# Kernel optimization log

Measured on AMD Instinct MI355X. Metric: run time of the kernel, lower is better.

Reference implementation:

```python
import jax, jax.numpy as jnp
import numpy as np

FORMULA_OH_SIZES = [20, 20, 20, 20, 20]
SPECT_BIN_N = 512


def layer_norm(x, g, b, eps=1e-5):
    m = jnp.mean(x, axis=-1, keepdims=True)
    v = jnp.var(x, axis=-1, keepdims=True)
    return (x - m) * jax.lax.rsqrt(v + eps) * g + b


def gru_cell(x, h, W_ih, W_hh, b_ih, b_hh):
    # torch.nn.GRUCell math
    gi = x @ W_ih.T + b_ih
    gh = h @ W_hh.T + b_hh
    i_r, i_z, i_n = jnp.split(gi, 3, axis=-1)
    h_r, h_z, h_n = jnp.split(gh, 3, axis=-1)
    r = jax.nn.sigmoid(i_r + h_r)
    z = jax.nn.sigmoid(i_z + h_z)
    n = jnp.tanh(i_n + r * h_n)
    return (1.0 - z) * n + z * h


def structured_one_hot(x, sizes, accum=True):
    # x: [N, len(sizes)] integer element counts -> concatenated (accumulated) one-hots
    outs = []
    for i, s in enumerate(sizes):
        v = jnp.clip(x[:, i].astype(jnp.int32), 0, s - 1)
        if accum:
            oh = (jnp.arange(s)[None, :] <= v[:, None]).astype(jnp.float32)  # thermometer
        else:
            oh = jax.nn.one_hot(v, s, dtype=jnp.float32)
        outs.append(oh)
    return jnp.concatenate(outs, axis=-1)


def setup_inputs():
    key = jax.random.key(0)
    ks = jax.random.split(key, 16)
    B, A, GF, HW, S, M = 16, 32, 128, 4, 4096, 8
    G = GF * HW                       # 512 = g_feat_in * highway_steps_n
    FE = sum(FORMULA_OH_SIZES)        # 100
    D = 512                           # internal_d
    vert_feat_in = jax.random.normal(ks[0], (B, A, GF, HW), jnp.float32)
    vert_mask_in = jnp.ones((B, A), jnp.float32)
    elem_id = jax.random.randint(ks[1], (B, A), 0, 5)
    vert_element_oh = jax.nn.one_hot(elem_id, 5, dtype=jnp.float32)
    adj_oh = jnp.zeros((B, A, A, 4), jnp.float32)  # unused by forward
    atom_subsets = jax.random.bernoulli(ks[2], 0.5, (B, S, A)).astype(jnp.float32)
    masses = jax.random.uniform(ks[3], (B, S, M), jnp.float32, 0.0, SPECT_BIN_N - 1.0)
    intens = jax.random.uniform(ks[4], (B, S, M), jnp.float32)
    atom_subsets_peaks = jnp.stack([masses, intens], axis=-1)

    def lin(k, o, i):
        return (jax.random.normal(k, (o, i), jnp.float32) / np.sqrt(i)).astype(jnp.float32)

    return dict(
        vert_feat_in=vert_feat_in, vert_mask_in=vert_mask_in,
        vert_element_oh=vert_element_oh, adj_oh=adj_oh,
        atom_subsets=atom_subsets, atom_subsets_peaks=atom_subsets_peaks,
        ln_sub_g=jnp.ones((G,), jnp.float32), ln_sub_b=jnp.zeros((G,), jnp.float32),
        W_ih=lin(ks[5], 3 * G, FE), W_hh=lin(ks[6], 3 * G, G),
        b_ih=jnp.zeros((3 * G,), jnp.float32), b_hh=jnp.zeros((3 * G,), jnp.float32),
        W1=lin(ks[7], D, G), b1=jnp.zeros((D,), jnp.float32),
        W2a=lin(ks[8], D, D), b2a=jnp.zeros((D,), jnp.float32),
        W2b=lin(ks[9], D, D), b2b=jnp.zeros((D,), jnp.float32),
        ln_pre_g=jnp.ones((D,), jnp.float32), ln_pre_b=jnp.zeros((D,), jnp.float32),
        Ws=lin(ks[10], 1, D), bs=jnp.zeros((1,), jnp.float32),
    )


def reference(vert_feat_in, vert_mask_in, vert_element_oh, adj_oh, atom_subsets,
              atom_subsets_peaks, ln_sub_g, ln_sub_b, W_ih, W_hh, b_ih, b_hh,
              W1, b1, W2a, b2a, W2b, b2b, ln_pre_g, ln_pre_b, Ws, bs):
    B, A, GF, HW = vert_feat_in.shape
    S = atom_subsets.shape[1]
    vf = vert_feat_in.reshape(B, A, GF * HW)                       # [B,A,G]
    masked_vf = vf * vert_mask_in[:, :, None]
    subs_m = atom_subsets * vert_mask_in[:, None, :]               # [B,S,A]
    swvs = jnp.einsum('bag,bsa->bsg', masked_vf, subs_m)           # [B,S,G]
    # per-subset element counts -> structured one-hot formula encoding
    counts = jnp.einsum('bae,bsa->bse', vert_element_oh, atom_subsets).astype(jnp.int32)
    pf_flat = structured_one_hot(counts.reshape(B * S, -1), FORMULA_OH_SIZES, accum=True)
    subset_size = jnp.sum(subs_m, axis=2) + 1e-4                   # [B,S]
    mean = swvs / subset_size[:, :, None]
    normed = layer_norm(mean, ln_sub_g, ln_sub_b)                  # [B,S,G]
    h = gru_cell(pf_flat, normed.reshape(B * S, -1), W_ih, W_hh, b_ih, b_hh)
    h = h.reshape(normed.shape)
    x = jax.nn.relu(h @ W1.T + b1)
    x = jax.nn.relu(x @ W2a.T + b2a)
    x = jax.nn.relu(x @ W2b.T + b2b)   # (extra F.relu in original is idempotent)
    x = layer_norm(x, ln_pre_g, ln_pre_b)
    scores = (x @ Ws.T + bs)[..., 0]                               # [B,S]
    probs = jax.nn.softmax(scores, axis=-1)
    # mass histogram: scatter intensity*prob into rounded-mass bins
    masses = atom_subsets_peaks[..., 0]                            # [B,S,M]
    intens = atom_subsets_peaks[..., 1]
    bins = jnp.clip(jnp.round(masses).astype(jnp.int32), 0, SPECT_BIN_N - 1)
    contrib = intens * probs[:, :, None]                           # [B,S,M]
    spect = jnp.zeros((B, SPECT_BIN_N), x.dtype).at[
        jnp.arange(B)[:, None], bins.reshape(B, -1)].add(contrib.reshape(B, -1))
    return (spect, probs)
```

## Files before the change

kernel.cpp:

```cpp
#include <hip/hip_runtime.h>
#include <math.h>

#define B_ 16
#define A_ 32
#define G_ 512
#define S_ 4096
#define M_ 8
#define BS_ 65536
#define KC_ 640
#define NG_ 1536

typedef _Float16 half8 __attribute__((ext_vector_type(8)));
typedef _Float16 half4v __attribute__((ext_vector_type(4)));
typedef _Float16 half2v __attribute__((ext_vector_type(2)));
typedef float floatx4 __attribute__((ext_vector_type(4)));

typedef const __attribute__((address_space(1))) void* gas_t;
typedef __attribute__((address_space(3))) void* las_t;

__device__ __forceinline__ float wave_sum_f(float v){
#pragma unroll
  for (int o = 32; o > 0; o >>= 1) v += __shfl_xor(v, o);
  return v;
}
__device__ __forceinline__ float wave_max_f(float v){
#pragma unroll
  for (int o = 32; o > 0; o >>= 1) v = fmaxf(v, __shfl_xor(v, o));
  return v;
}
__device__ __forceinline__ float sigmoidf_(float x){ return 1.f/(1.f+__expf(-x)); }
__device__ __forceinline__ float tanhf_(float x){ return 1.f - 2.f/(__expf(2.f*x)+1.f); }

__global__ __launch_bounds__(256) void k_cvt(const float* __restrict__ s,
                                             _Float16* __restrict__ d, int n){
  int i = (blockIdx.x*256 + threadIdx.x)*4;
  if (i >= n) return;
  float4 v = *(const float4*)(s+i);
  half4v o; o[0]=(_Float16)v.x; o[1]=(_Float16)v.y; o[2]=(_Float16)v.z; o[3]=(_Float16)v.w;
  *(half4v*)(d+i) = o;
}

__global__ __launch_bounds__(64) void k_buildw(const float* __restrict__ Whh,
                                               const float* __restrict__ Wih,
                                               _Float16* __restrict__ Wcat){
  int j = blockIdx.x;
  for (int p = threadIdx.x; p < KC_; p += 64){
    float v = 0.f;
    if (p < 512) v = Whh[(size_t)j*512 + p];
    else if (p < 612 && j < 1024) v = Wih[(size_t)j*100 + (p - 512)];
    Wcat[(size_t)j*KC_ + p] = (_Float16)v;
  }
}

__global__ __launch_bounds__(256) void k_pn(const float* __restrict__ Wih,
                                            float* __restrict__ Pn){
  int d = blockIdx.x*256 + threadIdx.x;
  if (d >= 512) return;
  const float* src = Wih + (size_t)(1024 + d)*100;
#pragma unroll
  for (int f = 0; f < 5; ++f){
    int off = f*20;
    float run = 0.f;
    for (int k = 0; k < 20; ++k){
      run += src[off + k];
      Pn[(size_t)(off + k)*512 + d] = run;
    }
  }
}

__global__ __launch_bounds__(256) void k_prep_mfma(
    const float* __restrict__ vf, const float* __restrict__ mask,
    const float* __restrict__ eoh, const float* __restrict__ subs,
    const float* __restrict__ ln_g, const float* __restrict__ ln_b,
    _Float16* __restrict__ Abuf, int* __restrict__ cpk){
  __shared__ _Float16 s_mvfT[G_*A_];
  __shared__ _Float16 s_sm[128*A_];
  __shared__ float s_m[A_];
  __shared__ float s_e[A_*5];
  __shared__ float s_ssum[128];
  __shared__ float s_red1[4][16];
  __shared__ float s_red2[4][16];
  int tid = threadIdx.x;
  int bx = blockIdx.x, b = blockIdx.y;
  int lane = tid & 63, w = tid >> 6;
  int q = lane >> 4, l15 = lane & 15;
  size_t row0 = (size_t)b*S_ + (size_t)bx*128;
  if (tid < A_)   s_m[tid] = mask[b*A_ + tid];
  if (tid < A_*5) s_e[tid] = eoh[b*A_*5 + tid];
  __syncthreads();
  {
    int p = tid & 15, gseg = tid >> 4;
    float mk0 = s_m[2*p], mk1 = s_m[2*p+1];
    const float* v0 = vf + ((size_t)b*A_ + 2*p)*G_ + gseg*32;
    const float* v1 = v0 + G_;
#pragma unroll
    for (int i = 0; i < 32; ++i){
      int g = gseg*32 + i;
      half2v h; h[0] = (_Float16)(v0[i]*mk0); h[1] = (_Float16)(v1[i]*mk1);
      *(half2v*)(s_mvfT + g*A_ + 2*p) = h;
    }
  }
  {
    int s = tid >> 1, hh = tid & 1;
    const float* sp = subs + (row0 + s)*A_ + hh*16;
#pragma unroll
    for (int i = 0; i < 16; i += 2){
      half2v h; h[0] = (_Float16)sp[i]; h[1] = (_Float16)sp[i+1];
      *(half2v*)(s_sm + s*A_ + hh*16 + i) = h;
    }
  }
  __syncthreads();
  if (tid < 128){
    int s = tid;
    float ssum = 0.f, c0=0.f, c1=0.f, c2=0.f, c3=0.f, c4=0.f;
#pragma unroll
    for (int a = 0; a < A_; ++a){
      float v = (float)s_sm[s*A_ + a];
      ssum += v * s_m[a];
      c0 += v * s_e[a*5+0]; c1 += v * s_e[a*5+1]; c2 += v * s_e[a*5+2];
      c3 += v * s_e[a*5+3]; c4 += v * s_e[a*5+4];
    }
    int cc[5];
    cc[0] = min(max((int)(c0+0.5f),0),19); cc[1] = min(max((int)(c1+0.5f),0),19);
    cc[2] = min(max((int)(c2+0.5f),0),19); cc[3] = min(max((int)(c3+0.5f),0),19);
    cc[4] = min(max((int)(c4+0.5f),0),19);
    cpk[row0 + s] = cc[0] | (cc[1]<<6) | (cc[2]<<12) | (cc[3]<<18) | (cc[4]<<24);
    s_ssum[s] = ssum;
    _Float16* dst = Abuf + (row0 + s)*KC_ + 512;
#pragma unroll
    for (int t = 0; t < 16; ++t){
      half8 hv;
#pragma unroll
      for (int u = 0; u < 8; ++u){
        int k = t*8 + u;
        float v = 0.f;
        if (k < 100){ int f = k/20, l = k - f*20; v = (l <= cc[f]) ? 1.f : 0.f; }
        hv[u] = (_Float16)v;
      }
      *(half8*)(dst + t*8) = hv;
    }
  }
  half8 bf[8]; float lng[8], lnb[8];
#pragma unroll
  for (int t = 0; t < 8; ++t){
    int g = w*128 + t*16 + l15;
    bf[t] = *(const half8*)(s_mvfT + g*A_ + q*8);
    lng[t] = ln_g[g]; lnb[t] = ln_b[g];
  }
  __syncthreads();
  for (int gi = 0; gi < 8; ++gi){
    half8 af = *(const half8*)(s_sm + (gi*16 + l15)*A_ + q*8);
    floatx4 c[8];
#pragma unroll
    for (int t = 0; t < 8; ++t){
      floatx4 z = {0.f, 0.f, 0.f, 0.f};
      c[t] = __builtin_amdgcn_mfma_f32_16x16x32_f16(af, bf[t], z, 0, 0, 0);
    }
    float p1[4] = {0.f,0.f,0.f,0.f}, p2[4] = {0.f,0.f,0.f,0.f};
#pragma unroll
    for (int t = 0; t < 8; ++t)
#pragma unroll
      for (int r = 0; r < 4; ++r){ float v = c[t][r]; p1[r] += v; p2[r] += v*v; }
#pragma unroll
    for (int off = 1; off < 16; off <<= 1)
#pragma unroll
      for (int r = 0; r < 4; ++r){
        p1[r] += __shfl_xor(p1[r], off);
        p2[r] += __shfl_xor(p2[r], off);
      }
    if (l15 == 0){
#pragma unroll
      for (int r = 0; r < 4; ++r){ s_red1[w][q*4+r] = p1[r]; s_red2[w][q*4+r] = p2[r]; }
    }
    __syncthreads();
#pragma unroll
    for (int r = 0; r < 4; ++r){
      int sl = gi*16 + q*4 + r;
      int rr = q*4 + r;
      float t1 = s_red1[0][rr] + s_red1[1][rr] + s_red1[2][rr] + s_red1[3][rr];
      float t2 = s_red2[0][rr] + s_red2[1][rr] + s_red2[2][rr] + s_red2[3][rr];
      float inv = 1.f/(s_ssum[sl] + 1e-4f);
      float mu = t1*inv*(1.f/512.f);
      float var = t2*inv*inv*(1.f/512.f) - mu*mu;
      float rs = rsqrtf(var + 1e-5f);
      _Float16* orow = Abuf + (row0 + sl)*KC_;
#pragma unroll
      for (int t = 0; t < 8; ++t){
        float o = (c[t][r]*inv - mu)*rs*lng[t] + lnb[t];
        orow[w*128 + t*16 + l15] = (_Float16)o;
      }
    }
    __syncthreads();
  }
}

__global__ __launch_bounds__(512) void k_gru_fused(
    const _Float16* __restrict__ Abuf, const _Float16* __restrict__ Wcat,
    const float* __restrict__ Pn, const float* __restrict__ bih,
    const float* __restrict__ bhh, const int* __restrict__ cpk,
    _Float16* __restrict__ H){
  __shared__ _Float16 smA[128*32];
  __shared__ _Float16 smB[192*32];
  int tid = threadIdx.x;
  int lane = tid & 63, wvid = tid >> 6;
  int wm = wvid & 1, wn = wvid >> 1;
  int q = lane >> 4, l15 = lane & 15;
  int mt = blockIdx.x*64 + (blockIdx.y >> 3);
  int dt = blockIdx.y & 7;
  int m0 = mt*128, n0 = dt*64;
  floatx4 acc[3][4] = {};
  int offA[4], offB[3];
#pragma unroll
  for (int i = 0; i < 4; ++i){
    int r = wm*64 + i*16 + l15;
    offA[i] = (r*4 + (q ^ ((r>>2)&3)))*8;
  }
#pragma unroll
  for (int g = 0; g < 3; ++g){
    int rb = g*64 + wn*16 + l15;
    offB[g] = (rb*4 + (q ^ ((rb>>2)&3)))*8;
  }
  const _Float16* gA;
  {
    int u = wvid*64 + lane;
    int r = u >> 2, c = (u & 3) ^ ((r >> 2) & 3);
    gA = Abuf + (size_t)(m0 + r)*KC_ + c*8;
  }
  const _Float16* gB0;
  {
    int u = wvid*64 + lane;
    int rb = u >> 2, c = (u & 3) ^ ((rb >> 2) & 3);
    int grow = (rb >> 6)*512 + n0 + (rb & 63);
    gB0 = Wcat + (size_t)grow*KC_ + c*8;
  }
  const _Float16* gB1 = nullptr;
  if (wvid < 4){
    int u = (8 + wvid)*64 + lane;
    int rb = u >> 2, c = (u & 3) ^ ((rb >> 2) & 3);
    int grow = (rb >> 6)*512 + n0 + (rb & 63);
    gB1 = Wcat + (size_t)grow*KC_ + c*8;
  }
  for (int kc = 0; kc < KC_; kc += 32){
    __builtin_amdgcn_global_load_lds((gas_t)(gA + kc), (las_t)(smA + wvid*512), 16, 0, 0);
    __builtin_amdgcn_global_load_lds((gas_t)(gB0 + kc), (las_t)(smB + wvid*512), 16, 0, 0);
    if (wvid < 4)
      __builtin_amdgcn_global_load_lds((gas_t)(gB1 + kc), (las_t)(smB + (8+wvid)*512), 16, 0, 0);
    __syncthreads();
    half8 af[4], bfv[3];
#pragma unroll
    for (int i = 0; i < 4; ++i) af[i] = *(const half8*)(smA + offA[i]);
#pragma unroll
    for (int g = 0; g < 3; ++g) bfv[g] = *(const half8*)(smB + offB[g]);
#pragma unroll
    for (int g = 0; g < 3; ++g)
#pragma unroll
      for (int i = 0; i < 4; ++i)
        acc[g][i] = __builtin_amdgcn_mfma_f32_16x16x32_f16(af[i], bfv[g], acc[g][i], 0, 0, 0);
    __syncthreads();
  }
  int d = n0 + wn*16 + l15;
  float br  = bih[d] + bhh[d];
  float bz  = bih[512+d] + bhh[512+d];
  float bnh = bhh[1024+d];
  float bni = bih[1024+d];
#pragma unroll
  for (int i = 0; i < 4; ++i){
#pragma unroll
    for (int r = 0; r < 4; ++r){
      int m = m0 + wm*64 + i*16 + q*4 + r;
      int cp = cpk[m];
      int k0 =  (cp      ) & 63;
      int k1 = ((cp >> 6 ) & 63) + 20;
      int k2 = ((cp >> 12) & 63) + 40;
      int k3 = ((cp >> 18) & 63) + 60;
      int k4 = ((cp >> 24) & 63) + 80;
      float in_ = bni + Pn[(size_t)k0*512 + d] + Pn[(size_t)k1*512 + d]
                + Pn[(size_t)k2*512 + d] + Pn[(size_t)k3*512 + d]
                + Pn[(size_t)k4*512 + d];
      float gr = acc[0][i][r] + br;
      float gz = acc[1][i][r] + bz;
      float hn = acc[2][i][r] + bnh;
      float rrv = sigmoidf_(gr);
      float zz  = sigmoidf_(gz);
      float nn  = tanhf_(in_ + rrv*hn);
      float hp = (float)Abuf[(size_t)m*KC_ + d];
      H[(size_t)m*G_ + d] = (_Float16)((1.f-zz)*nn + zz*hp);
    }
  }
}

__global__ __launch_bounds__(256) void k_gemm(
    const _Float16* __restrict__ A, const _Float16* __restrict__ W,
    const float* __restrict__ bias, _Float16* __restrict__ Out){
  __shared__ _Float16 smA[128*32];
  __shared__ _Float16 smB[128*32];
  int tid = threadIdx.x;
  int lane = tid & 63, wvid = tid >> 6;
  int wm = wvid & 1, wn = wvid >> 1;
  int q = lane >> 4, l15 = lane & 15;
  int mt = blockIdx.x*64 + (blockIdx.y >> 2);
  int nt = blockIdx.y & 3;
  int m0 = mt*128, n0 = nt*128;
  floatx4 acc[4][4] = {};
  int offA[4], offB[4];
#pragma unroll
  for (int i = 0; i < 4; ++i){
    int r = wm*64 + i*16 + l15;
    offA[i] = (r*4 + (q ^ ((r>>2)&3)))*8;
    int rb = wn*64 + i*16 + l15;
    offB[i] = (rb*4 + (q ^ ((rb>>2)&3)))*8;
  }
  int uA[2];
  const _Float16 *gA[2], *gB[2];
#pragma unroll
  for (int t = 0; t < 2; ++t){
    int seg = wvid*2 + t;
    int u = seg*64 + lane;
    int r = u >> 2, c = (u & 3) ^ ((r >> 2) & 3);
    uA[t] = seg;
    gA[t] = A + (size_t)(m0 + r)*G_ + c*8;
    gB[t] = W + (size_t)(n0 + r)*G_ + c*8;
  }
  for (int kc = 0; kc < G_; kc += 32){
#pragma unroll
    for (int t = 0; t < 2; ++t){
      __builtin_amdgcn_global_load_lds((gas_t)(gA[t] + kc), (las_t)(smA + uA[t]*512), 16, 0, 0);
      __builtin_amdgcn_global_load_lds((gas_t)(gB[t] + kc), (las_t)(smB + uA[t]*512), 16, 0, 0);
    }
    __syncthreads();
    half8 af[4], bfv[4];
#pragma unroll
    for (int i = 0; i < 4; ++i) af[i] = *(const half8*)(smA + offA[i]);
#pragma unroll
    for (int j = 0; j < 4; ++j) bfv[j] = *(const half8*)(smB + offB[j]);
#pragma unroll
    for (int i = 0; i < 4; ++i)
#pragma unroll
      for (int j = 0; j < 4; ++j)
        acc[i][j] = __builtin_amdgcn_mfma_f32_16x16x32_f16(af[i], bfv[j], acc[i][j], 0, 0, 0);
    __syncthreads();
  }
#pragma unroll
  for (int j = 0; j < 4; ++j){
    int n = n0 + wn*64 + j*16 + l15;
    float bv = bias[n];
#pragma unroll
    for (int i = 0; i < 4; ++i){
#pragma unroll
      for (int r = 0; r < 4; ++r){
        int m = m0 + wm*64 + i*16 + q*4 + r;
        Out[(size_t)m*G_ + n] = (_Float16)fmaxf(acc[i][j][r] + bv, 0.f);
      }
    }
  }
}

__global__ __launch_bounds__(256) void k_ln_score(
    const _Float16* __restrict__ X, const float* __restrict__ g,
    const float* __restrict__ bta, const float* __restrict__ Ws,
    const float* __restrict__ bs, float* __restrict__ scores){
  int tid = threadIdx.x, lane = tid & 63, wv = tid >> 6;
  size_t row0 = (size_t)blockIdx.x*32 + wv*8;
  int e0 = lane*8;
  float wv_[8], gv[8], bv[8];
  *(float4*)(wv_ ) = *(const float4*)(Ws + e0);
  *(float4*)(wv_+4) = *(const float4*)(Ws + e0 + 4);
  *(float4*)(gv  ) = *(const float4*)(g + e0);
  *(float4*)(gv+4) = *(const float4*)(g + e0 + 4);
  *(float4*)(bv  ) = *(const float4*)(bta + e0);
  *(float4*)(bv+4) = *(const float4*)(bta + e0 + 4);
  float bsv = bs[0];
  for (int rr = 0; rr < 8; ++rr){
    size_t row = row0 + rr;
    half8 hx = *(const half8*)(X + row*G_ + e0);
    float xv[8];
#pragma unroll
    for (int t = 0; t < 8; ++t) xv[t] = (float)hx[t];
    float s1 = 0.f, s2 = 0.f;
#pragma unroll
    for (int t = 0; t < 8; ++t){ s1 += xv[t]; s2 += xv[t]*xv[t]; }
    s1 = wave_sum_f(s1); s2 = wave_sum_f(s2);
    float mu = s1*(1.f/512.f);
    float var = s2*(1.f/512.f) - mu*mu;
    float rs = rsqrtf(var + 1e-5f);
    float sc = 0.f;
#pragma unroll
    for (int t = 0; t < 8; ++t) sc += ((xv[t]-mu)*rs*gv[t] + bv[t])*wv_[t];
    sc = wave_sum_f(sc);
    if (lane == 0) scores[row] = sc + bsv;
  }
}

__global__ __launch_bounds__(256) void k_softmax(
    const float* __restrict__ scores, float* __restrict__ probs){
  __shared__ float red[4];
  int b = blockIdx.x, tid = threadIdx.x, lane = tid & 63, wv = tid >> 6;
  const float* sp = scores + (size_t)b*S_;
  float mx = -1e30f;
  for (int i = tid; i < S_; i += 256) mx = fmaxf(mx, sp[i]);
  mx = wave_max_f(mx);
  if (lane == 0) red[wv] = mx;
  __syncthreads();
  mx = fmaxf(fmaxf(red[0], red[1]), fmaxf(red[2], red[3]));
  __syncthreads();
  float sum = 0.f;
  for (int i = tid; i < S_; i += 256) sum += __expf(sp[i]-mx);
  sum = wave_sum_f(sum);
  if (lane == 0) red[wv] = sum;
  __syncthreads();
  sum = red[0]+red[1]+red[2]+red[3];
  float inv = 1.f/sum;
  for (int i = tid; i < S_; i += 256)
    probs[(size_t)b*S_ + i] = __expf(sp[i]-mx)*inv;
}

__global__ __launch_bounds__(256) void k_spect(
    const float* __restrict__ peaks, const float* __restrict__ probs,
    float* __restrict__ spect){
  __shared__ float bins[512];
  int b = blockIdx.x, tid = threadIdx.x;
  bins[tid] = 0.f; bins[tid+256] = 0.f;
  __syncthreads();
  for (int i = tid; i < S_*M_; i += 256){
    int s = i >> 3, m = i & 7;
    const float* pk = peaks + (((size_t)b*S_ + s)*M_ + m)*2;
    float mass = pk[0], inten = pk[1];
    float p = probs[(size_t)b*S_ + s];
    int bin = (int)rintf(mass);
    bin = min(max(bin, 0), 511);
    atomicAdd(&bins[bin], inten*p);
  }
  __syncthreads();
  spect[(size_t)b*512 + tid]       = bins[tid];
  spect[(size_t)b*512 + tid + 256] = bins[tid+256];
}

extern "C" void kernel_launch(void* const* d_in, const int* in_sizes, int n_in,
                              void* d_out, int out_size, void* d_ws, size_t ws_size,
                              hipStream_t stream) {
  const float* vf       = (const float*)d_in[0];
  const float* mask     = (const float*)d_in[1];
  const float* eoh      = (const float*)d_in[2];
  const float* subs     = (const float*)d_in[4];
  const float* peaks    = (const float*)d_in[5];
  const float* ln_sub_g = (const float*)d_in[6];
  const float* ln_sub_b = (const float*)d_in[7];
  const float* W_ih     = (const float*)d_in[8];
  const float* W_hh     = (const float*)d_in[9];
  const float* b_ih     = (const float*)d_in[10];
  const float* b_hh     = (const float*)d_in[11];
  const float* W1       = (const float*)d_in[12];
  const float* b1       = (const float*)d_in[13];
  const float* W2a      = (const float*)d_in[14];
  const float* b2a      = (const float*)d_in[15];
  const float* W2b      = (const float*)d_in[16];
  const float* b2b      = (const float*)d_in[17];
  const float* ln_pre_g = (const float*)d_in[18];
  const float* ln_pre_b = (const float*)d_in[19];
  const float* Ws       = (const float*)d_in[20];
  const float* bs       = (const float*)d_in[21];
  float* out = (float*)d_out;
  float* probs_out = out + (size_t)B_*512;

  char* w = (char*)d_ws;
  float* Pn = (float*)w;         w += (size_t)100*512*4;
  int*   cpk = (int*)w;          w += (size_t)BS_*4;
  float* scores = (float*)w;     w += (size_t)BS_*4;
  _Float16* Wcat = (_Float16*)w; w += (size_t)NG_*KC_*2;
  _Float16* W1h  = (_Float16*)w; w += (size_t)G_*G_*2;
  _Float16* W2ah = (_Float16*)w; w += (size_t)G_*G_*2;
  _Float16* W2bh = (_Float16*)w; w += (size_t)G_*G_*2;
  _Float16* Abuf = (_Float16*)w; w += (size_t)BS_*KC_*2;
  _Float16* bufh0 = (_Float16*)w;
  _Float16* bufh1 = Abuf;

  k_cvt<<<(G_*G_/4+255)/256, 256, 0, stream>>>(W1,  W1h,  G_*G_);
  k_cvt<<<(G_*G_/4+255)/256, 256, 0, stream>>>(W2a, W2ah, G_*G_);
  k_cvt<<<(G_*G_/4+255)/256, 256, 0, stream>>>(W2b, W2bh, G_*G_);
  k_buildw<<<NG_, 64, 0, stream>>>(W_hh, W_ih, Wcat);
  k_pn<<<2, 256, 0, stream>>>(W_ih, Pn);
  k_prep_mfma<<<dim3(S_/128, B_), 256, 0, stream>>>(vf, mask, eoh, subs,
                                                    ln_sub_g, ln_sub_b, Abuf, cpk);
  k_gru_fused<<<dim3(8, 512), 512, 0, stream>>>(Abuf, Wcat, Pn, b_ih, b_hh,
                                                cpk, bufh0);
  k_gemm<<<dim3(8, 256), 256, 0, stream>>>(bufh0, W1h,  b1,  bufh1);
  k_gemm<<<dim3(8, 256), 256, 0, stream>>>(bufh1, W2ah, b2a, bufh0);
  k_gemm<<<dim3(8, 256), 256, 0, stream>>>(bufh0, W2bh, b2b, bufh1);
  k_ln_score<<<BS_/32, 256, 0, stream>>>(bufh1, ln_pre_g, ln_pre_b, Ws, bs, scores);
  k_softmax<<<B_, 256, 0, stream>>>(scores, probs_out);
  k_spect<<<B_, 256, 0, stream>>>(peaks, probs_out, out);
}
```

Measured before the change: 541.6 us.

## Switch GRU and MLP GEMMs to 32x32x16 MFMA with larger per-wave tiles

Replaces the 16x16x32 MFMA tiling in the fused GRU kernel and the MLP GEMM kernel with 32x32x16 instructions, so each wave now computes 64x32 or 64x64 output tiles. The LDS swizzle is changed to suit the new fragment read pattern. The GRU kernel drops from 512 to 256 threads per block, with each wave loading more segments. The aim is fewer LDS fragment reads per FLOP and higher MFMA throughput, at the cost of more accumulator registers per wave and a changed epilogue row mapping.

```diff
diff --git a/kernel.cpp b/kernel.cpp
--- a/kernel.cpp
+++ b/kernel.cpp
@@ -14,6 +14,7 @@
 typedef _Float16 half4v __attribute__((ext_vector_type(4)));
 typedef _Float16 half2v __attribute__((ext_vector_type(2)));
 typedef float floatx4 __attribute__((ext_vector_type(4)));
+typedef float floatx16 __attribute__((ext_vector_type(16)));
 
 typedef const __attribute__((address_space(1))) void* gas_t;
 typedef __attribute__((address_space(3))) void* las_t;
@@ -194,7 +195,7 @@
   }
 }
 
-__global__ __launch_bounds__(512) void k_gru_fused(
+__global__ __launch_bounds__(256) void k_gru_fused(
     const _Float16* __restrict__ Abuf, const _Float16* __restrict__ Wcat,
     const float* __restrict__ Pn, const float* __restrict__ bih,
     const float* __restrict__ bhh, const int* __restrict__ cpk,
@@ -204,70 +205,81 @@
   int tid = threadIdx.x;
   int lane = tid & 63, wvid = tid >> 6;
   int wm = wvid & 1, wn = wvid >> 1;
-  int q = lane >> 4, l15 = lane & 15;
+  int l31 = lane & 31, lhi = lane >> 5;
   int mt = blockIdx.x*64 + (blockIdx.y >> 3);
   int dt = blockIdx.y & 7;
   int m0 = mt*128, n0 = dt*64;
-  floatx4 acc[3][4] = {};
-  int offA[4], offB[3];
-#pragma unroll
-  for (int i = 0; i < 4; ++i){
-    int r = wm*64 + i*16 + l15;
-    offA[i] = (r*4 + (q ^ ((r>>2)&3)))*8;
+  floatx16 acc[3][2] = {};
+  int offA[2][2], offB[3][2];
+#pragma unroll
+  for (int mi = 0; mi < 2; ++mi){
+    int r = wm*64 + mi*32 + l31;
+#pragma unroll
+    for (int c = 0; c < 2; ++c)
+      offA[mi][c] = (r*4 + ((c*2 + lhi) ^ ((r>>1)&3)))*8;
   }
 #pragma unroll
   for (int g = 0; g < 3; ++g){
-    int rb = g*64 + wn*16 + l15;
-    offB[g] = (rb*4 + (q ^ ((rb>>2)&3)))*8;
-  }
-  const _Float16* gA;
-  {
-    int u = wvid*64 + lane;
-    int r = u >> 2, c = (u & 3) ^ ((r >> 2) & 3);
-    gA = Abuf + (size_t)(m0 + r)*KC_ + c*8;
-  }
-  const _Float16* gB0;
-  {
-    int u = wvid*64 + lane;
-    int rb = u >> 2, c = (u & 3) ^ ((rb >> 2) & 3);
+    int rb = g*64 + wn*32 + l31;
+#pragma unroll
+    for (int c = 0; c < 2; ++c)
+      offB[g][c] = (rb*4 + ((c*2 + lhi) ^ ((rb>>1)&3)))*8;
+  }
+  const _Float16* gA[2]; int sAo[2];
+#pragma unroll
+  for (int t = 0; t < 2; ++t){
+    int seg = wvid + t*4;
+    int u = seg*64 + lane;
+    int r = u >> 2, c = (u & 3) ^ ((r >> 1) & 3);
+    gA[t] = Abuf + (size_t)(m0 + r)*KC_ + c*8;
+    sAo[t] = seg*512;
+  }
+  const _Float16* gB[3]; int sBo[3];
+#pragma unroll
+  for (int t = 0; t < 3; ++t){
+    int seg = wvid*3 + t;
+    int u = seg*64 + lane;
+    int rb = u >> 2, c = (u & 3) ^ ((rb >> 1) & 3);
     int grow = (rb >> 6)*512 + n0 + (rb & 63);
-    gB0 = Wcat + (size_t)grow*KC_ + c*8;
-  }
-  const _Float16* gB1 = nullptr;
-  if (wvid < 4){
-    int u = (8 + wvid)*64 + lane;
-    int rb = u >> 2, c = (u & 3) ^ ((rb >> 2) & 3);
-    int grow = (rb >> 6)*512 + n0 + (rb & 63);
-    gB1 = Wcat + (size_t)grow*KC_ + c*8;
+    gB[t] = Wcat + (size_t)grow*KC_ + c*8;
+    sBo[t] = seg*512;
   }
   for (int kc = 0; kc < KC_; kc += 32){
-    __builtin_amdgcn_global_load_lds((gas_t)(gA + kc), (las_t)(smA + wvid*512), 16, 0, 0);
-    __builtin_amdgcn_global_load_lds((gas_t)(gB0 + kc), (las_t)(smB + wvid*512), 16, 0, 0);
-    if (wvid < 4)
-      __builtin_amdgcn_global_load_lds((gas_t)(gB1 + kc), (las_t)(smB + (8+wvid)*512), 16, 0, 0);
+#pragma unroll
+    for (int t = 0; t < 2; ++t)
+      __builtin_amdgcn_global_load_lds((gas_t)(gA[t] + kc), (las_t)(smA + sAo[t]), 16, 0, 0);
+#pragma unroll
+    for (int t = 0; t < 3; ++t)
+      __builtin_amdgcn_global_load_lds((gas_t)(gB[t] + kc), (las_t)(smB + sBo[t]), 16, 0, 0);
     __syncthreads();
-    half8 af[4], bfv[3];
-#pragma unroll
-    for (int i = 0; i < 4; ++i) af[i] = *(const half8*)(smA + offA[i]);
-#pragma unroll
-    for (int g = 0; g < 3; ++g) bfv[g] = *(const half8*)(smB + offB[g]);
+    half8 af[2][2], bfv[3][2];
+#pragma unroll
+    for (int mi = 0; mi < 2; ++mi)
+#pragma unroll
+      for (int c = 0; c < 2; ++c) af[mi][c] = *(const half8*)(smA + offA[mi][c]);
 #pragma unroll
     for (int g = 0; g < 3; ++g)
 #pragma unroll
-      for (int i = 0; i < 4; ++i)
-        acc[g][i] = __builtin_amdgcn_mfma_f32_16x16x32_f16(af[i], bfv[g], acc[g][i], 0, 0, 0);
+      for (int c = 0; c < 2; ++c) bfv[g][c] = *(const half8*)(smB + offB[g][c]);
+#pragma unroll
+    for (int g = 0; g < 3; ++g)
+#pragma unroll
+      for (int mi = 0; mi < 2; ++mi)
+#pragma unroll
+        for (int c = 0; c < 2; ++c)
+          acc[g][mi] = __builtin_amdgcn_mfma_f32_32x32x16_f16(af[mi][c], bfv[g][c], acc[g][mi], 0, 0, 0);
     __syncthreads();
   }
-  int d = n0 + wn*16 + l15;
+  int d = n0 + wn*32 + l31;
   float br  = bih[d] + bhh[d];
   float bz  = bih[512+d] + bhh[512+d];
   float bnh = bhh[1024+d];
   float bni = bih[1024+d];
 #pragma unroll
-  for (int i = 0; i < 4; ++i){
-#pragma unroll
-    for (int r = 0; r < 4; ++r){
-      int m = m0 + wm*64 + i*16 + q*4 + r;
+  for (int mi = 0; mi < 2; ++mi){
+#pragma unroll
+    for (int rr = 0; rr < 16; ++rr){
+      int m = m0 + wm*64 + mi*32 + (rr&3) + 8*(rr>>2) + 4*lhi;
       int cp = cpk[m];
       int k0 =  (cp      ) & 63;
       int k1 = ((cp >> 6 ) & 63) + 20;
@@ -277,9 +289,9 @@
       float in_ = bni + Pn[(size_t)k0*512 + d] + Pn[(size_t)k1*512 + d]
                 + Pn[(size_t)k2*512 + d] + Pn[(size_t)k3*512 + d]
                 + Pn[(size_t)k4*512 + d];
-      float gr = acc[0][i][r] + br;
-      float gz = acc[1][i][r] + bz;
-      float hn = acc[2][i][r] + bnh;
+      float gr = acc[0][mi][rr] + br;
+      float gz = acc[1][mi][rr] + bz;
+      float hn = acc[2][mi][rr] + bnh;
       float rrv = sigmoidf_(gr);
       float zz  = sigmoidf_(gz);
       float nn  = tanhf_(in_ + rrv*hn);
@@ -297,59 +309,66 @@
   int tid = threadIdx.x;
   int lane = tid & 63, wvid = tid >> 6;
   int wm = wvid & 1, wn = wvid >> 1;
-  int q = lane >> 4, l15 = lane & 15;
+  int l31 = lane & 31, lhi = lane >> 5;
   int mt = blockIdx.x*64 + (blockIdx.y >> 2);
   int nt = blockIdx.y & 3;
   int m0 = mt*128, n0 = nt*128;
-  floatx4 acc[4][4] = {};
-  int offA[4], offB[4];
-#pragma unroll
-  for (int i = 0; i < 4; ++i){
-    int r = wm*64 + i*16 + l15;
-    offA[i] = (r*4 + (q ^ ((r>>2)&3)))*8;
-    int rb = wn*64 + i*16 + l15;
-    offB[i] = (rb*4 + (q ^ ((rb>>2)&3)))*8;
-  }
-  int uA[2];
-  const _Float16 *gA[2], *gB[2];
+  floatx16 acc[2][2] = {};
+  int offA[2][2], offB[2][2];
+#pragma unroll
+  for (int mi = 0; mi < 2; ++mi){
+    int r = wm*64 + mi*32 + l31;
+    int rb = wn*64 + mi*32 + l31;
+#pragma unroll
+    for (int c = 0; c < 2; ++c){
+      offA[mi][c] = (r*4 + ((c*2 + lhi) ^ ((r>>1)&3)))*8;
+      offB[mi][c] = (rb*4 + ((c*2 + lhi) ^ ((rb>>1)&3)))*8;
+    }
+  }
+  const _Float16 *gA[2], *gB[2]; int uo[2];
 #pragma unroll
   for (int t = 0; t < 2; ++t){
     int seg = wvid*2 + t;
     int u = seg*64 + lane;
-    int r = u >> 2, c = (u & 3) ^ ((r >> 2) & 3);
-    uA[t] = seg;
+    int r = u >> 2, c = (u & 3) ^ ((r >> 1) & 3);
+    uo[t] = seg*512;
     gA[t] = A + (size_t)(m0 + r)*G_ + c*8;
     gB[t] = W + (size_t)(n0 + r)*G_ + c*8;
   }
   for (int kc = 0; kc < G_; kc += 32){
 #pragma unroll
     for (int t = 0; t < 2; ++t){
-      __builtin_amdgcn_global_load_lds((gas_t)(gA[t] + kc), (las_t)(smA + uA[t]*512), 16, 0, 0);
-      __builtin_amdgcn_global_load_lds((gas_t)(gB[t] + kc), (las_t)(smB + uA[t]*512), 16, 0, 0);
+      __builtin_amdgcn_global_load_lds((gas_t)(gA[t] + kc), (las_t)(smA + uo[t]), 16, 0, 0);
+      __builtin_amdgcn_global_load_lds((gas_t)(gB[t] + kc), (las_t)(smB + uo[t]), 16, 0, 0);
     }
     __syncthreads();
-    half8 af[4], bfv[4];
-#pragma unroll
-    for (int i = 0; i < 4; ++i) af[i] = *(const half8*)(smA + offA[i]);
-#pragma unroll
-    for (int j = 0; j < 4; ++j) bfv[j] = *(const half8*)(smB + offB[j]);
-#pragma unroll
-    for (int i = 0; i < 4; ++i)
-#pragma unroll
-      for (int j = 0; j < 4; ++j)
-        acc[i][j] = __builtin_amdgcn_mfma_f32_16x16x32_f16(af[i], bfv[j], acc[i][j], 0, 0, 0);
+    half8 af[2][2], bfv[2][2];
+#pragma unroll
+    for (int mi = 0; mi < 2; ++mi)
+#pragma unroll
+      for (int c = 0; c < 2; ++c){
+        af[mi][c] = *(const half8*)(smA + offA[mi][c]);
+        bfv[mi][c] = *(const half8*)(smB + offB[mi][c]);
+      }
+#pragma unroll
+    for (int mi = 0; mi < 2; ++mi)
+#pragma unroll
+      for (int nj = 0; nj < 2; ++nj)
+#pragma unroll
+        for (int c = 0; c < 2; ++c)
+          acc[mi][nj] = __builtin_amdgcn_mfma_f32_32x32x16_f16(af[mi][c], bfv[nj][c], acc[mi][nj], 0, 0, 0);
     __syncthreads();
   }
 #pragma unroll
-  for (int j = 0; j < 4; ++j){
-    int n = n0 + wn*64 + j*16 + l15;
+  for (int nj = 0; nj < 2; ++nj){
+    int n = n0 + wn*64 + nj*32 + l31;
     float bv = bias[n];
 #pragma unroll
-    for (int i = 0; i < 4; ++i){
-#pragma unroll
-      for (int r = 0; r < 4; ++r){
-        int m = m0 + wm*64 + i*16 + q*4 + r;
-        Out[(size_t)m*G_ + n] = (_Float16)fmaxf(acc[i][j][r] + bv, 0.f);
+    for (int mi = 0; mi < 2; ++mi){
+#pragma unroll
+      for (int rr = 0; rr < 16; ++rr){
+        int m = m0 + wm*64 + mi*32 + (rr&3) + 8*(rr>>2) + 4*lhi;
+        Out[(size_t)m*G_ + n] = (_Float16)fmaxf(acc[mi][nj][rr] + bv, 0.f);
       }
     }
   }
@@ -481,7 +500,7 @@
   k_pn<<<2, 256, 0, stream>>>(W_ih, Pn);
   k_prep_mfma<<<dim3(S_/128, B_), 256, 0, stream>>>(vf, mask, eoh, subs,
                                                     ln_sub_g, ln_sub_b, Abuf, cpk);
-  k_gru_fused<<<dim3(8, 512), 512, 0, stream>>>(Abuf, Wcat, Pn, b_ih, b_hh,
+  k_gru_fused<<<dim3(8, 512), 256, 0, stream>>>(Abuf, Wcat, Pn, b_ih, b_hh,
                                                 cpk, bufh0);
   k_gemm<<<dim3(8, 256), 256, 0, stream>>>(bufh0, W1h,  b1,  bufh1);
   k_gemm<<<dim3(8, 256), 256, 0, stream>>>(bufh1, W2ah, b2a, bufh0);
```

New measurement: 567.2 us. 1.05x slower.

## Replace one-hot input GEMM columns with prefix-sum table lookups for all gates

Applied to the files above, without the earlier changes.

The GRU input contribution from the thermometer one-hot formula encoding was folded into the GEMM as 128 extra K columns (K=640). It is now computed for all three gates by gathering five entries from per-gate prefix-sum tables of W_ih. This shrinks the GEMM K dimension to 512, drops the one-hot writes in the prep kernel, and replaces the weight-concat kernel with a plain conversion. In exchange the epilogue does 15 scattered table loads per output element instead of 5, which may add cache pressure.

```diff
diff --git a/kernel.cpp b/kernel.cpp
--- a/kernel.cpp
+++ b/kernel.cpp
@@ -7,7 +7,6 @@
 #define S_ 4096
 #define M_ 8
 #define BS_ 65536
-#define KC_ 640
 #define NG_ 1536
 
 typedef _Float16 half8 __attribute__((ext_vector_type(8)));
@@ -40,30 +39,20 @@
   *(half4v*)(d+i) = o;
 }
 
-__global__ __launch_bounds__(64) void k_buildw(const float* __restrict__ Whh,
-                                               const float* __restrict__ Wih,
-                                               _Float16* __restrict__ Wcat){
-  int j = blockIdx.x;
-  for (int p = threadIdx.x; p < KC_; p += 64){
-    float v = 0.f;
-    if (p < 512) v = Whh[(size_t)j*512 + p];
-    else if (p < 612 && j < 1024) v = Wih[(size_t)j*100 + (p - 512)];
-    Wcat[(size_t)j*KC_ + p] = (_Float16)v;
-  }
-}
-
-__global__ __launch_bounds__(256) void k_pn(const float* __restrict__ Wih,
-                                            float* __restrict__ Pn){
-  int d = blockIdx.x*256 + threadIdx.x;
-  if (d >= 512) return;
-  const float* src = Wih + (size_t)(1024 + d)*100;
+__global__ __launch_bounds__(256) void k_pt(const float* __restrict__ Wih,
+                                            float* __restrict__ Pt){
+  int j = blockIdx.x*256 + threadIdx.x;
+  if (j >= 1536) return;
+  int g = j >> 9, d = j & 511;
+  const float* src = Wih + (size_t)j*100;
+  float* dst = Pt + (size_t)g*100*512 + d;
 #pragma unroll
   for (int f = 0; f < 5; ++f){
     int off = f*20;
     float run = 0.f;
     for (int k = 0; k < 20; ++k){
       run += src[off + k];
-      Pn[(size_t)(off + k)*512 + d] = run;
+      dst[(size_t)(off + k)*512] = run;
     }
   }
 }
@@ -126,19 +115,6 @@
     cc[4] = min(max((int)(c4+0.5f),0),19);
     cpk[row0 + s] = cc[0] | (cc[1]<<6) | (cc[2]<<12) | (cc[3]<<18) | (cc[4]<<24);
     s_ssum[s] = ssum;
-    _Float16* dst = Abuf + (row0 + s)*KC_ + 512;
-#pragma unroll
-    for (int t = 0; t < 16; ++t){
-      half8 hv;
-#pragma unroll
-      for (int u = 0; u < 8; ++u){
-        int k = t*8 + u;
-        float v = 0.f;
-        if (k < 100){ int f = k/20, l = k - f*20; v = (l <= cc[f]) ? 1.f : 0.f; }
-        hv[u] = (_Float16)v;
-      }
-      *(half8*)(dst + t*8) = hv;
-    }
   }
   half8 bf[8]; float lng[8], lnb[8];
 #pragma unroll
@@ -183,7 +159,7 @@
       float mu = t1*inv*(1.f/512.f);
       float var = t2*inv*inv*(1.f/512.f) - mu*mu;
       float rs = rsqrtf(var + 1e-5f);
-      _Float16* orow = Abuf + (row0 + sl)*KC_;
+      _Float16* orow = Abuf + (row0 + sl)*G_;
 #pragma unroll
       for (int t = 0; t < 8; ++t){
         float o = (c[t][r]*inv - mu)*rs*lng[t] + lnb[t];
@@ -195,8 +171,8 @@
 }
 
 __global__ __launch_bounds__(512) void k_gru_fused(
-    const _Float16* __restrict__ Abuf, const _Float16* __restrict__ Wcat,
-    const float* __restrict__ Pn, const float* __restrict__ bih,
+    const _Float16* __restrict__ Abuf, const _Float16* __restrict__ W16,
+    const float* __restrict__ Pt, const float* __restrict__ bih,
     const float* __restrict__ bhh, const int* __restrict__ cpk,
     _Float16* __restrict__ H){
   __shared__ _Float16 smA[128*32];
@@ -224,23 +200,23 @@
   {
     int u = wvid*64 + lane;
     int r = u >> 2, c = (u & 3) ^ ((r >> 2) & 3);
-    gA = Abuf + (size_t)(m0 + r)*KC_ + c*8;
+    gA = Abuf + (size_t)(m0 + r)*G_ + c*8;
   }
   const _Float16* gB0;
   {
     int u = wvid*64 + lane;
     int rb = u >> 2, c = (u & 3) ^ ((rb >> 2) & 3);
     int grow = (rb >> 6)*512 + n0 + (rb & 63);
-    gB0 = Wcat + (size_t)grow*KC_ + c*8;
+    gB0 = W16 + (size_t)grow*G_ + c*8;
   }
   const _Float16* gB1 = nullptr;
   if (wvid < 4){
     int u = (8 + wvid)*64 + lane;
     int rb = u >> 2, c = (u & 3) ^ ((rb >> 2) & 3);
     int grow = (rb >> 6)*512 + n0 + (rb & 63);
-    gB1 = Wcat + (size_t)grow*KC_ + c*8;
-  }
-  for (int kc = 0; kc < KC_; kc += 32){
+    gB1 = W16 + (size_t)grow*G_ + c*8;
+  }
+  for (int kc = 0; kc < G_; kc += 32){
     __builtin_amdgcn_global_load_lds((gas_t)(gA + kc), (las_t)(smA + wvid*512), 16, 0, 0);
     __builtin_amdgcn_global_load_lds((gas_t)(gB0 + kc), (las_t)(smB + wvid*512), 16, 0, 0);
     if (wvid < 4)
@@ -259,6 +235,9 @@
     __syncthreads();
   }
   int d = n0 + wn*16 + l15;
+  const float* Pr = Pt + d;
+  const float* Pz = Pt + 100*512 + d;
+  const float* Pn = Pt + 200*512 + d;
   float br  = bih[d] + bhh[d];
   float bz  = bih[512+d] + bhh[512+d];
   float bnh = bhh[1024+d];
@@ -269,21 +248,22 @@
     for (int r = 0; r < 4; ++r){
       int m = m0 + wm*64 + i*16 + q*4 + r;
       int cp = cpk[m];
-      int k0 =  (cp      ) & 63;
-      int k1 = ((cp >> 6 ) & 63) + 20;
-      int k2 = ((cp >> 12) & 63) + 40;
-      int k3 = ((cp >> 18) & 63) + 60;
-      int k4 = ((cp >> 24) & 63) + 80;
-      float in_ = bni + Pn[(size_t)k0*512 + d] + Pn[(size_t)k1*512 + d]
-                + Pn[(size_t)k2*512 + d] + Pn[(size_t)k3*512 + d]
-                + Pn[(size_t)k4*512 + d];
-      float gr = acc[0][i][r] + br;
-      float gz = acc[1][i][r] + bz;
+      int k0 = ((cp      ) & 63)*512;
+      int k1 = (((cp >> 6 ) & 63) + 20)*512;
+      int k2 = (((cp >> 12) & 63) + 40)*512;
+      int k3 = (((cp >> 18) & 63) + 60)*512;
+      int k4 = (((cp >> 24) & 63) + 80)*512;
+      float sr = Pr[k0]+Pr[k1]+Pr[k2]+Pr[k3]+Pr[k4];
+      float sz = Pz[k0]+Pz[k1]+Pz[k2]+Pz[k3]+Pz[k4];
+      float sn = Pn[k0]+Pn[k1]+Pn[k2]+Pn[k3]+Pn[k4];
+      float gr = acc[0][i][r] + br + sr;
+      float gz = acc[1][i][r] + bz + sz;
       float hn = acc[2][i][r] + bnh;
+      float in_ = bni + sn;
       float rrv = sigmoidf_(gr);
       float zz  = sigmoidf_(gz);
       float nn  = tanhf_(in_ + rrv*hn);
-      float hp = (float)Abuf[(size_t)m*KC_ + d];
+      float hp = (float)Abuf[(size_t)m*G_ + d];
       H[(size_t)m*G_ + d] = (_Float16)((1.f-zz)*nn + zz*hp);
     }
   }
@@ -463,25 +443,25 @@
   float* probs_out = out + (size_t)B_*512;
 
   char* w = (char*)d_ws;
-  float* Pn = (float*)w;         w += (size_t)100*512*4;
+  float* Pt = (float*)w;         w += (size_t)3*100*512*4;
   int*   cpk = (int*)w;          w += (size_t)BS_*4;
   float* scores = (float*)w;     w += (size_t)BS_*4;
-  _Float16* Wcat = (_Float16*)w; w += (size_t)NG_*KC_*2;
+  _Float16* W3h  = (_Float16*)w; w += (size_t)NG_*G_*2;
   _Float16* W1h  = (_Float16*)w; w += (size_t)G_*G_*2;
   _Float16* W2ah = (_Float16*)w; w += (size_t)G_*G_*2;
   _Float16* W2bh = (_Float16*)w; w += (size_t)G_*G_*2;
-  _Float16* Abuf = (_Float16*)w; w += (size_t)BS_*KC_*2;
+  _Float16* Abuf = (_Float16*)w; w += (size_t)BS_*G_*2;
   _Float16* bufh0 = (_Float16*)w;
   _Float16* bufh1 = Abuf;
 
+  k_cvt<<<(NG_*G_/4+255)/256, 256, 0, stream>>>(W_hh, W3h, NG_*G_);
   k_cvt<<<(G_*G_/4+255)/256, 256, 0, stream>>>(W1,  W1h,  G_*G_);
   k_cvt<<<(G_*G_/4+255)/256, 256, 0, stream>>>(W2a, W2ah, G_*G_);
   k_cvt<<<(G_*G_/4+255)/256, 256, 0, stream>>>(W2b, W2bh, G_*G_);
-  k_buildw<<<NG_, 64, 0, stream>>>(W_hh, W_ih, Wcat);
-  k_pn<<<2, 256, 0, stream>>>(W_ih, Pn);
+  k_pt<<<6, 256, 0, stream>>>(W_ih, Pt);
   k_prep_mfma<<<dim3(S_/128, B_), 256, 0, stream>>>(vf, mask, eoh, subs,
                                                     ln_sub_g, ln_sub_b, Abuf, cpk);
-  k_gru_fused<<<dim3(8, 512), 512, 0, stream>>>(Abuf, Wcat, Pn, b_ih, b_hh,
+  k_gru_fused<<<dim3(8, 512), 512, 0, stream>>>(Abuf, W3h, Pt, b_ih, b_hh,
                                                 cpk, bufh0);
   k_gemm<<<dim3(8, 256), 256, 0, stream>>>(bufh0, W1h,  b1,  bufh1);
   k_gemm<<<dim3(8, 256), 256, 0, stream>>>(bufh1, W2ah, b2a, bufh0);
```

Result: slower. 556.9 us (+2.8%).
